# Kernel optimization log

Hardware: AMD Instinct MI355X
Metric: run time of the kernel (lower is better)

The kernel has to match this reference:

```python
import jax, jax.numpy as jnp
import numpy as np

N_NODES = 100000
N_EDGES = 3200000
INPUT_DIM = 16
HIDDEN_DIM = 8


def setup_inputs() -> dict:
    key = jax.random.key(0)
    k1, k2, k3, k4 = jax.random.split(key, 4)
    x = jax.random.normal(k1, (N_NODES, INPUT_DIM), dtype=jnp.float32)
    edge_index = jax.random.randint(k2, (2, N_EDGES), 0, N_NODES, dtype=jnp.int64)
    # PyTorch Linear default init: U(-1/sqrt(fan_in), 1/sqrt(fan_in)); scaled normal is fine for a reference
    W1 = jax.random.normal(k3, (2 * INPUT_DIM, HIDDEN_DIM), dtype=jnp.float32) / np.sqrt(2 * INPUT_DIM)
    b1 = jnp.zeros((HIDDEN_DIM,), dtype=jnp.float32)
    W2 = jax.random.normal(k4, (HIDDEN_DIM, 1), dtype=jnp.float32) / np.sqrt(HIDDEN_DIM)
    b2 = jnp.zeros((1,), dtype=jnp.float32)
    return {"x": x, "edge_index": edge_index, "W1": W1, "b1": b1, "W2": W2, "b2": b2}


def reference(x, edge_index, W1, b1, W2, b2):
    row, col = edge_index[0], edge_index[1]
    # B = cat([x[col], x[row]], dim=-1).detach()  -> [E, 2*input_dim]
    B = jax.lax.stop_gradient(jnp.concatenate([x[col], x[row]], axis=-1))
    h = jnp.tanh(B @ W1 + b1)            # [E, hidden_dim]
    out = jax.nn.sigmoid(h @ W2 + b2)    # [E, 1]
    return out
```

## Files before the change

### kernel.cpp

```cpp
#include <hip/hip_runtime.h>
#include <hip/hip_fp16.h>

#define IN_DIM 16
#define HID 8

typedef int   v4i __attribute__((ext_vector_type(4)));
typedef float v4f __attribute__((ext_vector_type(4)));

__device__ __forceinline__ float fast_tanh(float z) {
    float e = __expf(2.0f * z);
    return 1.0f - 2.0f * __builtin_amdgcn_rcpf(e + 1.0f);
}

__global__ __launch_bounds__(256) void node_pre(
    const float* __restrict__ x, const float* __restrict__ W1,
    const float* __restrict__ b1, __half* __restrict__ uv, int n_nodes)
{
    __shared__ float sW[2 * IN_DIM * HID];
    __shared__ float sb[HID];
    int t = threadIdx.x;
    if (t < 2 * IN_DIM * HID) sW[t] = W1[t];
    if (t < HID) sb[t] = b1[t];
    __syncthreads();
    int n = blockIdx.x * 256 + t;
    if (n >= n_nodes) return;

    const float4* xp = (const float4*)(x + (size_t)n * IN_DIM);
    float xr[IN_DIM];
    float4 a;
    a = xp[0]; xr[0]=a.x;  xr[1]=a.y;  xr[2]=a.z;  xr[3]=a.w;
    a = xp[1]; xr[4]=a.x;  xr[5]=a.y;  xr[6]=a.z;  xr[7]=a.w;
    a = xp[2]; xr[8]=a.x;  xr[9]=a.y;  xr[10]=a.z; xr[11]=a.w;
    a = xp[3]; xr[12]=a.x; xr[13]=a.y; xr[14]=a.z; xr[15]=a.w;

    float au[HID], av[HID];
    #pragma unroll
    for (int j = 0; j < HID; j++) { au[j] = sb[j]; av[j] = 0.0f; }
    #pragma unroll
    for (int k = 0; k < IN_DIM; k++) {
        #pragma unroll
        for (int j = 0; j < HID; j++) {
            au[j] = fmaf(xr[k], sW[k * HID + j], au[j]);
            av[j] = fmaf(xr[k], sW[(IN_DIM + k) * HID + j], av[j]);
        }
    }
    union { __half2 h[4]; float4 f; } pu, pv;
    #pragma unroll
    for (int i = 0; i < 4; i++) {
        pu.h[i] = __floats2half2_rn(au[2*i], au[2*i+1]);
        pv.h[i] = __floats2half2_rn(av[2*i], av[2*i+1]);
    }
    float4* o = (float4*)(uv + (size_t)n * 16);
    o[0] = pu.f;
    o[1] = pv.f;
}

__device__ __forceinline__ void gather8_sc0(
    const float4* a0, const float4* a1, const float4* a2, const float4* a3,
    const float4* a4, const float4* a5, const float4* a6, const float4* a7,
    float4& r0, float4& r1, float4& r2, float4& r3,
    float4& r4, float4& r5, float4& r6, float4& r7)
{
    asm volatile(
        "global_load_dwordx4 %0, %8, off sc0\n\t"
        "global_load_dwordx4 %1, %9, off sc0\n\t"
        "global_load_dwordx4 %2, %10, off sc0\n\t"
        "global_load_dwordx4 %3, %11, off sc0\n\t"
        "global_load_dwordx4 %4, %12, off sc0\n\t"
        "global_load_dwordx4 %5, %13, off sc0\n\t"
        "global_load_dwordx4 %6, %14, off sc0\n\t"
        "global_load_dwordx4 %7, %15, off sc0\n\t"
        "s_waitcnt vmcnt(0)"
        : "=&v"(r0), "=&v"(r1), "=&v"(r2), "=&v"(r3),
          "=&v"(r4), "=&v"(r5), "=&v"(r6), "=&v"(r7)
        : "v"(a0), "v"(a1), "v"(a2), "v"(a3),
          "v"(a4), "v"(a5), "v"(a6), "v"(a7)
        : "memory");
}

__device__ __forceinline__ float edge_eval(float4 uf, float4 vf,
                                           const float* sw2, float sb2)
{
    union { float4 f; __half2 h[4]; } U, V;
    U.f = uf; V.f = vf;
    float s = sb2;
    #pragma unroll
    for (int i = 0; i < 4; i++) {
        float2 a = __half22float2(U.h[i]);
        float2 b = __half22float2(V.h[i]);
        s = fmaf(fast_tanh(a.x + b.x), sw2[2*i],   s);
        s = fmaf(fast_tanh(a.y + b.y), sw2[2*i+1], s);
    }
    return __builtin_amdgcn_rcpf(1.0f + __expf(-s));
}

__global__ __launch_bounds__(256) void edge_k(
    const int* __restrict__ idx, const __half* __restrict__ uv,
    const float* __restrict__ W2, const float* __restrict__ b2,
    float* __restrict__ out, int n_edges)
{
    __shared__ float sw2[HID];
    __shared__ float sb2;
    int t = threadIdx.x;
    if (t < HID) sw2[t] = W2[t];
    if (t == 0) sb2 = b2[0];
    __syncthreads();
    float lb2 = sb2;

    long e0 = ((long)blockIdx.x * 256 + t) * 4;
    const float4* uvp = (const float4*)uv;
    if (e0 + 4 <= n_edges) {
        v4i rows = __builtin_nontemporal_load((const v4i*)(idx + e0));
        v4i cols = __builtin_nontemporal_load((const v4i*)(idx + n_edges + e0));

        float4 u0, u1, u2, u3, w0, w1, w2, w3;
        gather8_sc0(uvp + 2*(size_t)cols.x,     uvp + 2*(size_t)cols.y,
                    uvp + 2*(size_t)cols.z,     uvp + 2*(size_t)cols.w,
                    uvp + 2*(size_t)rows.x + 1, uvp + 2*(size_t)rows.y + 1,
                    uvp + 2*(size_t)rows.z + 1, uvp + 2*(size_t)rows.w + 1,
                    u0, u1, u2, u3, w0, w1, w2, w3);

        v4f r;
        r.x = edge_eval(u0, w0, sw2, lb2);
        r.y = edge_eval(u1, w1, sw2, lb2);
        r.z = edge_eval(u2, w2, sw2, lb2);
        r.w = edge_eval(u3, w3, sw2, lb2);
        __builtin_nontemporal_store(r, (v4f*)(out + e0));
    } else {
        for (long e = e0; e < n_edges; e++) {
            int row = idx[e];
            int col = idx[n_edges + e];
            out[e] = edge_eval(uvp[2*(size_t)col], uvp[2*(size_t)row + 1], sw2, lb2);
        }
    }
}

extern "C" void kernel_launch(void* const* d_in, const int* in_sizes, int n_in,
                              void* d_out, int out_size, void* d_ws, size_t ws_size,
                              hipStream_t stream) {
    const float* x  = (const float*)d_in[0];
    const int*   idx = (const int*)d_in[1];
    const float* W1 = (const float*)d_in[2];
    const float* b1 = (const float*)d_in[3];
    const float* W2 = (const float*)d_in[4];
    const float* b2 = (const float*)d_in[5];
    float* out = (float*)d_out;

    int n_nodes = in_sizes[0] / IN_DIM;
    int n_edges = in_sizes[1] / 2;

    __half* uv = (__half*)d_ws;

    node_pre<<<(n_nodes + 255) / 256, 256, 0, stream>>>(x, W1, b1, uv, n_nodes);
    int epb = 256 * 4;
    edge_k<<<(n_edges + epb - 1) / epb, 256, 0, stream>>>(idx, uv, W2, b2, out, n_edges);
}
```

Measured before the change: 117.8 us.

## Process eight edges per thread with staged gathers and exp2-folded activations

Each thread now handles two groups of four edges and issues all sixteen random uv gathers at once. It waits only for the first half before evaluating the first group, so the second group's loads overlap with compute. Separately, the log2(e) scale factors are folded into W1/b1 and W2/b2, so tanh and sigmoid use raw exp2 instead of __expf with extra multiplies. The change raises memory-level parallelism per thread and halves the grid size, at the cost of higher VGPR pressure and possibly lower occupancy. The pre-scaled fp16 node values are also somewhat larger in magnitude.

```diff
diff --git a/kernel.cpp b/kernel.cpp
--- a/kernel.cpp
+++ b/kernel.cpp
@@ -3,14 +3,13 @@
 
 #define IN_DIM 16
 #define HID 8
+#define C1   2.8853900817779268f
+#define NL2E 1.4426950408889634f
 
 typedef int   v4i __attribute__((ext_vector_type(4)));
 typedef float v4f __attribute__((ext_vector_type(4)));
 
-__device__ __forceinline__ float fast_tanh(float z) {
-    float e = __expf(2.0f * z);
-    return 1.0f - 2.0f * __builtin_amdgcn_rcpf(e + 1.0f);
-}
+__device__ __forceinline__ float exp2_raw(float x) { return __builtin_amdgcn_exp2f(x); }
 
 __global__ __launch_bounds__(256) void node_pre(
     const float* __restrict__ x, const float* __restrict__ W1,
@@ -19,8 +18,8 @@
     __shared__ float sW[2 * IN_DIM * HID];
     __shared__ float sb[HID];
     int t = threadIdx.x;
-    if (t < 2 * IN_DIM * HID) sW[t] = W1[t];
-    if (t < HID) sb[t] = b1[t];
+    if (t < 2 * IN_DIM * HID) sW[t] = W1[t] * C1;
+    if (t < HID) sb[t] = b1[t] * C1;
     __syncthreads();
     int n = blockIdx.x * 256 + t;
     if (n >= n_nodes) return;
@@ -53,6 +52,26 @@
     float4* o = (float4*)(uv + (size_t)n * 16);
     o[0] = pu.f;
     o[1] = pv.f;
+}
+
+__device__ __forceinline__ float edge_eval(float4 uf, float4 vf,
+                                           const float* sw2, float sb2)
+{
+    union { float4 f; __half2 h[4]; } U, V;
+    U.f = uf; V.f = vf;
+    float s = sb2;
+    #pragma unroll
+    for (int i = 0; i < 4; i++) {
+        float2 a = __half22float2(U.h[i]);
+        float2 b = __half22float2(V.h[i]);
+        float e0 = exp2_raw(a.x + b.x);
+        float e1 = exp2_raw(a.y + b.y);
+        float t0 = 1.0f - 2.0f * __builtin_amdgcn_rcpf(e0 + 1.0f);
+        float t1 = 1.0f - 2.0f * __builtin_amdgcn_rcpf(e1 + 1.0f);
+        s = fmaf(t0, sw2[2*i],   s);
+        s = fmaf(t1, sw2[2*i+1], s);
+    }
+    return __builtin_amdgcn_rcpf(1.0f + exp2_raw(s));
 }
 
 __device__ __forceinline__ void gather8_sc0(
@@ -78,20 +97,12 @@
         : "memory");
 }
 
-__device__ __forceinline__ float edge_eval(float4 uf, float4 vf,
-                                           const float* sw2, float sb2)
-{
-    union { float4 f; __half2 h[4]; } U, V;
-    U.f = uf; V.f = vf;
-    float s = sb2;
-    #pragma unroll
-    for (int i = 0; i < 4; i++) {
-        float2 a = __half22float2(U.h[i]);
-        float2 b = __half22float2(V.h[i]);
-        s = fmaf(fast_tanh(a.x + b.x), sw2[2*i],   s);
-        s = fmaf(fast_tanh(a.y + b.y), sw2[2*i+1], s);
-    }
-    return __builtin_amdgcn_rcpf(1.0f + __expf(-s));
+__device__ __forceinline__ void edge_scalar(long e, const int* idx, long n_edges,
+    const float4* uvp, const float* sw2, float lb2, float* __restrict__ out)
+{
+    int r = idx[e];
+    int c = idx[n_edges + e];
+    out[e] = edge_eval(uvp[2*(size_t)c], uvp[2*(size_t)r + 1], sw2, lb2);
 }
 
 __global__ __launch_bounds__(256) void edge_k(
@@ -102,36 +113,97 @@
     __shared__ float sw2[HID];
     __shared__ float sb2;
     int t = threadIdx.x;
-    if (t < HID) sw2[t] = W2[t];
-    if (t == 0) sb2 = b2[0];
+    if (t < HID) sw2[t] = W2[t] * -NL2E;
+    if (t == 0) sb2 = b2[0] * -NL2E;
     __syncthreads();
     float lb2 = sb2;
 
-    long e0 = ((long)blockIdx.x * 256 + t) * 4;
     const float4* uvp = (const float4*)uv;
-    if (e0 + 4 <= n_edges) {
-        v4i rows = __builtin_nontemporal_load((const v4i*)(idx + e0));
-        v4i cols = __builtin_nontemporal_load((const v4i*)(idx + n_edges + e0));
-
-        float4 u0, u1, u2, u3, w0, w1, w2, w3;
-        gather8_sc0(uvp + 2*(size_t)cols.x,     uvp + 2*(size_t)cols.y,
-                    uvp + 2*(size_t)cols.z,     uvp + 2*(size_t)cols.w,
-                    uvp + 2*(size_t)rows.x + 1, uvp + 2*(size_t)rows.y + 1,
-                    uvp + 2*(size_t)rows.z + 1, uvp + 2*(size_t)rows.w + 1,
-                    u0, u1, u2, u3, w0, w1, w2, w3);
-
-        v4f r;
-        r.x = edge_eval(u0, w0, sw2, lb2);
-        r.y = edge_eval(u1, w1, sw2, lb2);
-        r.z = edge_eval(u2, w2, sw2, lb2);
-        r.w = edge_eval(u3, w3, sw2, lb2);
-        __builtin_nontemporal_store(r, (v4f*)(out + e0));
+    long base = (long)blockIdx.x * 2048;
+    long eA = base + (long)t * 4;
+    long eB = eA + 1024;
+
+    if (eB + 4 <= n_edges) {
+        v4i rA = __builtin_nontemporal_load((const v4i*)(idx + eA));
+        v4i cA = __builtin_nontemporal_load((const v4i*)(idx + n_edges + eA));
+        v4i rB = __builtin_nontemporal_load((const v4i*)(idx + eB));
+        v4i cB = __builtin_nontemporal_load((const v4i*)(idx + n_edges + eB));
+
+        float4 uA0, uA1, uA2, uA3, wA0, wA1, wA2, wA3;
+        float4 uB0, uB1, uB2, uB3, wB0, wB1, wB2, wB3;
+        asm volatile(
+            "global_load_dwordx4 %0, %16, off sc0\n\t"
+            "global_load_dwordx4 %1, %17, off sc0\n\t"
+            "global_load_dwordx4 %2, %18, off sc0\n\t"
+            "global_load_dwordx4 %3, %19, off sc0\n\t"
+            "global_load_dwordx4 %4, %20, off sc0\n\t"
+            "global_load_dwordx4 %5, %21, off sc0\n\t"
+            "global_load_dwordx4 %6, %22, off sc0\n\t"
+            "global_load_dwordx4 %7, %23, off sc0\n\t"
+            "global_load_dwordx4 %8, %24, off sc0\n\t"
+            "global_load_dwordx4 %9, %25, off sc0\n\t"
+            "global_load_dwordx4 %10, %26, off sc0\n\t"
+            "global_load_dwordx4 %11, %27, off sc0\n\t"
+            "global_load_dwordx4 %12, %28, off sc0\n\t"
+            "global_load_dwordx4 %13, %29, off sc0\n\t"
+            "global_load_dwordx4 %14, %30, off sc0\n\t"
+            "global_load_dwordx4 %15, %31, off sc0"
+            : "=&v"(uA0), "=&v"(uA1), "=&v"(uA2), "=&v"(uA3),
+              "=&v"(wA0), "=&v"(wA1), "=&v"(wA2), "=&v"(wA3),
+              "=&v"(uB0), "=&v"(uB1), "=&v"(uB2), "=&v"(uB3),
+              "=&v"(wB0), "=&v"(wB1), "=&v"(wB2), "=&v"(wB3)
+            : "v"(uvp + 2*(size_t)cA.x),     "v"(uvp + 2*(size_t)cA.y),
+              "v"(uvp + 2*(size_t)cA.z),     "v"(uvp + 2*(size_t)cA.w),
+              "v"(uvp + 2*(size_t)rA.x + 1), "v"(uvp + 2*(size_t)rA.y + 1),
+              "v"(uvp + 2*(size_t)rA.z + 1), "v"(uvp + 2*(size_t)rA.w + 1),
+              "v"(uvp + 2*(size_t)cB.x),     "v"(uvp + 2*(size_t)cB.y),
+              "v"(uvp + 2*(size_t)cB.z),     "v"(uvp + 2*(size_t)cB.w),
+              "v"(uvp + 2*(size_t)rB.x + 1), "v"(uvp + 2*(size_t)rB.y + 1),
+              "v"(uvp + 2*(size_t)rB.z + 1), "v"(uvp + 2*(size_t)rB.w + 1)
+            : "memory");
+
+        asm volatile("s_waitcnt vmcnt(8)" ::: "memory");
+        __builtin_amdgcn_sched_barrier(0);
+
+        v4f ra;
+        ra.x = edge_eval(uA0, wA0, sw2, lb2);
+        ra.y = edge_eval(uA1, wA1, sw2, lb2);
+        ra.z = edge_eval(uA2, wA2, sw2, lb2);
+        ra.w = edge_eval(uA3, wA3, sw2, lb2);
+
+        asm volatile("s_waitcnt vmcnt(0)" ::: "memory");
+        __builtin_amdgcn_sched_barrier(0);
+
+        v4f rb;
+        rb.x = edge_eval(uB0, wB0, sw2, lb2);
+        rb.y = edge_eval(uB1, wB1, sw2, lb2);
+        rb.z = edge_eval(uB2, wB2, sw2, lb2);
+        rb.w = edge_eval(uB3, wB3, sw2, lb2);
+
+        __builtin_nontemporal_store(ra, (v4f*)(out + eA));
+        __builtin_nontemporal_store(rb, (v4f*)(out + eB));
     } else {
-        for (long e = e0; e < n_edges; e++) {
-            int row = idx[e];
-            int col = idx[n_edges + e];
-            out[e] = edge_eval(uvp[2*(size_t)col], uvp[2*(size_t)row + 1], sw2, lb2);
+        if (eA + 4 <= n_edges) {
+            v4i rows = __builtin_nontemporal_load((const v4i*)(idx + eA));
+            v4i cols = __builtin_nontemporal_load((const v4i*)(idx + n_edges + eA));
+            float4 u0, u1, u2, u3, w0, w1, w2, w3;
+            gather8_sc0(uvp + 2*(size_t)cols.x,     uvp + 2*(size_t)cols.y,
+                        uvp + 2*(size_t)cols.z,     uvp + 2*(size_t)cols.w,
+                        uvp + 2*(size_t)rows.x + 1, uvp + 2*(size_t)rows.y + 1,
+                        uvp + 2*(size_t)rows.z + 1, uvp + 2*(size_t)rows.w + 1,
+                        u0, u1, u2, u3, w0, w1, w2, w3);
+            v4f r;
+            r.x = edge_eval(u0, w0, sw2, lb2);
+            r.y = edge_eval(u1, w1, sw2, lb2);
+            r.z = edge_eval(u2, w2, sw2, lb2);
+            r.w = edge_eval(u3, w3, sw2, lb2);
+            __builtin_nontemporal_store(r, (v4f*)(out + eA));
+        } else {
+            for (long e = eA; e < n_edges && e < eA + 4; ++e)
+                edge_scalar(e, idx, n_edges, uvp, sw2, lb2, out);
         }
+        for (long e = eB; e < n_edges && e < eB + 4; ++e)
+            edge_scalar(e, idx, n_edges, uvp, sw2, lb2, out);
     }
 }
 
@@ -152,6 +224,6 @@
     __half* uv = (__half*)d_ws;
 
     node_pre<<<(n_nodes + 255) / 256, 256, 0, stream>>>(x, W1, b1, uv, n_nodes);
-    int epb = 256 * 4;
+    int epb = 256 * 8;
     edge_k<<<(n_edges + epb - 1) / epb, 256, 0, stream>>>(idx, uv, W2, b2, out, n_edges);
 }
```

After: 119.2 us. About the same (+1.2%).
